# Kernel tuning notes

Measured on AMD Instinct MI355X. Metric: run time of the kernel, lower is better.

The kernel has to match this reference:

```python
import jax, jax.numpy as jnp
import numpy as np

K = 3      # kernel_size
PAD = 1    # padding


def _bilinear_gather(x, py, px, mask):
    """Modulated bilinear sampling (DCNv2 / torchvision semantics, zero padding).
    x:   [B,C,H,W]; py,px: [B,KK,H,W] float sample coords; mask: [B,KK,H,W].
    Returns [B,C,KK,H,W]."""
    B, C, H, W = x.shape
    KK = py.shape[1]
    y0f = jnp.floor(py); x0f = jnp.floor(px)
    y0 = y0f.astype(jnp.int32); x0 = x0f.astype(jnp.int32)
    wy1 = py - y0f; wx1 = px - x0f
    wy0 = 1.0 - wy1; wx0 = 1.0 - wx1
    x_flat = x.reshape(B, C, H * W)

    def corner(iy, ix, wgt):
        valid = (iy >= 0) & (iy < H) & (ix >= 0) & (ix < W)
        idx = (jnp.clip(iy, 0, H - 1) * W + jnp.clip(ix, 0, W - 1)).reshape(B, -1)
        g = jax.vmap(lambda xb, ib: jnp.take(xb, ib, axis=1))(x_flat, idx)
        g = g.reshape(B, C, KK, H, W)
        return g * (wgt * valid.astype(x.dtype))[:, None]

    val = (corner(y0, x0, wy0 * wx0)
           + corner(y0, x0 + 1, wy0 * wx1)
           + corner(y0 + 1, x0, wy1 * wx0)
           + corner(y0 + 1, x0 + 1, wy1 * wx1))
    return val * mask[:, None]


def reference(x, w_offset, b_offset, w_dcn):
    B, C, H, W = x.shape
    KK = K * K
    # offset/mask conv (stride 1, same padding)
    om = jax.lax.conv_general_dilated(
        x, w_offset, (1, 1), [(PAD, PAD), (PAD, PAD)],
        dimension_numbers=('NCHW', 'OIHW', 'NCHW')) + b_offset[None, :, None, None]
    o1, o2, m = om[:, :KK], om[:, KK:2 * KK], om[:, 2 * KK:]
    # module concatenates [o1, o2]; torchvision interprets channels as interleaved (dy, dx) pairs
    offset = jnp.concatenate([o1, o2], axis=1)          # [B, 2*KK, H, W]
    dy = offset[:, 0::2]                                # [B, KK, H, W]
    dx = offset[:, 1::2]
    mask = jax.nn.sigmoid(m)
    # base sampling grid per kernel tap
    kr = jnp.arange(K, dtype=x.dtype)
    ky = jnp.repeat(kr, K)                              # [KK]
    kx = jnp.tile(kr, K)
    by = jnp.arange(H, dtype=x.dtype)[:, None]          # [H,1]
    bx = jnp.arange(W, dtype=x.dtype)[None, :]          # [1,W]
    py = by[None, None] - PAD + ky[None, :, None, None] + dy
    px = bx[None, None] - PAD + kx[None, :, None, None] + dx
    val = _bilinear_gather(x, py, px, mask)             # [B,C,KK,H,W]
    w = w_dcn.reshape(w_dcn.shape[0], C, KK)            # [Cout, Cin, KK]
    return jnp.einsum('bckhw,ock->bohw', val, w)


def setup_inputs() -> dict:
    key = jax.random.key(0)
    k1, k2, k3, k4 = jax.random.split(key, 4)
    B, C_in, C_out, H, W = 8, 64, 64, 128, 128
    KK = K * K
    x = jax.random.normal(k1, (B, C_in, H, W), dtype=jnp.float32)
    # small nonzero offset weights so sampling positions are perturbed (module inits to 0)
    w_offset = jax.random.normal(k2, (3 * KK, C_in, K, K), dtype=jnp.float32) * 0.01
    b_offset = jax.random.normal(k3, (3 * KK,), dtype=jnp.float32) * 0.01
    fan_in = C_in * KK
    w_dcn = jax.random.normal(k4, (C_out, C_in, K, K), dtype=jnp.float32) / np.sqrt(fan_in)
    return {"x": x, "w_offset": w_offset, "b_offset": b_offset, "w_dcn": w_dcn}
```

## Files before the change

### kernel.cpp

```cpp
#include <hip/hip_runtime.h>
#include <math.h>

#define BATCH 8
#define CIN 64
#define COUT 64
#define HH 128
#define WW 128
#define HW (HH*WW)
#define TPX 64
#define KDIM 576
#define NR 5
#define NC 69
#define NSLOT (NR*NC)
#define NITEM (NSLOT*8)

typedef __attribute__((ext_vector_type(8))) short short8;
typedef __attribute__((ext_vector_type(4))) float f32x4;
typedef __attribute__((ext_vector_type(4))) unsigned int u32x4;
typedef _Float16 h2   __attribute__((ext_vector_type(2)));
typedef _Float16 h8   __attribute__((ext_vector_type(8)));

__device__ __forceinline__ short f2h(float f) {
    union { _Float16 h; short s; } u;
    u.h = (_Float16)f;
    return u.s;
}

__global__ void __launch_bounds__(256) prep_kernel(const float* __restrict__ x,
                                                   unsigned short* __restrict__ xT,
                                                   const float* __restrict__ w_dcn,
                                                   const float* __restrict__ w_off,
                                                   unsigned short* __restrict__ wt2,
                                                   unsigned short* __restrict__ wtoff2) {
    if (blockIdx.x < 4096) {
        int idx = blockIdx.x * 256 + threadIdx.x;
        int c8 = idx & 7;
        int w  = (idx >> 3) & 127;
        int h  = (idx >> 10) & 127;
        int b  = idx >> 17;
        const float* xp = x + (((size_t)(b * 64 + c8 * 8) * 128 + h) * 128 + w);
        short8 o;
#pragma unroll
        for (int j = 0; j < 8; ++j)
            o[j] = f2h(xp[(size_t)j * HW]);
        *(short8*)(xT + (size_t)idx * 8) = o;
        return;
    }
    int gid = (blockIdx.x - 4096) * 256 + threadIdx.x;
    if (gid < 72 * 64) {
        int frag = gid >> 6, lane = gid & 63;
        int kf = frag >> 3, s = (frag >> 2) & 1, m = frag & 3;
        int o = m * 16 + (lane & 15);
        int cb = s * 32 + (lane >> 4) * 8;
        short8 v;
#pragma unroll
        for (int j = 0; j < 8; ++j)
            v[j] = f2h(w_dcn[(o * 64 + cb + j) * 9 + kf]);
        *(short8*)(wt2 + (size_t)gid * 8) = v;
    } else {
        int g2 = gid - 72 * 64;
        if (g2 < 36 * 64) {
            int frag = g2 >> 6, lane = g2 & 63;
            int kk = frag >> 1, m = frag & 1;
            int kf = kk >> 1;
            int o = m * 16 + (lane & 15);
            int cb = (kk & 1) * 32 + (lane >> 4) * 8;
            short8 v;
#pragma unroll
            for (int j = 0; j < 8; ++j)
                v[j] = (o < 27) ? f2h(w_off[(o * 64 + cb + j) * 9 + kf]) : (short)0;
            *(short8*)(wtoff2 + (size_t)g2 * 8) = v;
        }
    }
}

#define LOAD_CORNERS(KF)                                                    \
    do {                                                                    \
        u32x4 e = *(const u32x4*)(s_geo8 + (size_t)(pxl * 9 + (KF)) * 16);  \
        int msk = (int)e.w >> 31;            \
        oow |= (e.w >> 31) << (KF);                                         \
        unsigned u0 = e.x & ~msk, u1 = e.y & ~msk;                          \
        union { unsigned u; h2 h; } c0_, c1_;                               \
        c0_.u = u0; c1_.u = u1;                                             \
        W0 = (h2){c0_.h.x, c0_.h.x}; W1 = (h2){c0_.h.y, c0_.h.y};           \
        W2 = (h2){c1_.h.x, c1_.h.x}; W3 = (h2){c1_.h.y, c1_.h.y};           \
        int base = (int)(e.z & ~msk);                                       \
        int sw00 = (int)(e.w & 0x70u);                                      \
        int sw01 = (int)((e.w >> 8) & 0x70u);                               \
        int sw10 = (int)((e.w >> 16) & 0x70u);                              \
        int sw11 = (int)((e.w >> 24) & 0x70u);                              \
        int q40 = g4 << 4;                                                  \
        int q41 = 64 + q40;                                                 \
        V0 = *(const h8*)(s_x + base + (q40 ^ sw00));                       \
        V1 = *(const h8*)(s_x + base + 128 + (q40 ^ sw01));                 \
        V2 = *(const h8*)(s_x + base + 8832 + (q40 ^ sw10));                \
        V3 = *(const h8*)(s_x + base + 8960 + (q40 ^ sw11));                \
        V4 = *(const h8*)(s_x + base + (q41 ^ sw00));                       \
        V5 = *(const h8*)(s_x + base + 128 + (q41 ^ sw01));                 \
        V6 = *(const h8*)(s_x + base + 8832 + (q41 ^ sw10));                \
        V7 = *(const h8*)(s_x + base + 8960 + (q41 ^ sw11));                \
    } while (0)

__global__ void __launch_bounds__(256, 3) fused_dcn_kernel(
        const unsigned short* __restrict__ xT,
        const unsigned short* __restrict__ wtoff2,
        const float* __restrict__ b_off,
        const unsigned short* __restrict__ wt2,
        float* __restrict__ out) {
    __shared__ char  s_x[NSLOT * 128];
    __shared__ float s_geo[TPX * 36];
    char* s_geo8 = (char*)s_geo;

    int t = threadIdx.x;
    int blk0 = blockIdx.x;
    int blk = (blk0 & 7) * 256 + (blk0 >> 3);
    int b = blk >> 8;
    int rem = blk & 255;
    int h = rem >> 1;
    int w0 = (rem & 1) << 6;

    int lane = t & 63;
    int wv = t >> 6;
    int l15 = lane & 15;
    int g4 = lane >> 4;
    int pxl = wv * 16 + l15;
    int wg = w0 + pxl;

    const unsigned short* xTb = xT + (size_t)b * HW * 64;

    {
        short8 v[11];
        int cs[11], cl[11];
#pragma unroll
        for (int it = 0; it < 11; ++it) {
            int i = it * 256 + t;
            if (i < NITEM) {
                int c_slot = i >> 3;
                cl[it] = i & 7;
                int r5 = c_slot / NC;
                int c  = c_slot - r5 * NC;
                cs[it] = c_slot;
                int row_src = min(max(h - 2 + r5, 0), 127);
                int col_src = min(max(w0 - 2 + c, 0), 127);
                v[it] = *(const short8*)(xTb + ((size_t)row_src * 128 + col_src) * 64 + cl[it] * 8);
            }
        }
#pragma unroll
        for (int it = 0; it < 11; ++it) {
            int i = it * 256 + t;
            if (i < NITEM) {
                int c_slot = cs[it];
                int r5 = c_slot / NC;
                int c = c_slot - r5 * NC;
                int baddr = c_slot * 128 + ((cl[it] ^ (c & 7) ^ r5) << 4);
                *(short8*)(s_x + baddr) = v[it];
            }
        }
    }
    __syncthreads();

    {
        f32x4 ca0 = {0.f, 0.f, 0.f, 0.f};
        f32x4 ca1 = {0.f, 0.f, 0.f, 0.f};
#pragma unroll
        for (int kk = 0; kk < 18; ++kk) {
            int kf = kk >> 1;
            int ky = kf / 3, kx = kf % 3;
            int cq = (kk & 1) * 4 + g4;
            int row = h - 1 + ky;
            int col = wg - 1 + kx;
            int cc = pxl + 1 + kx;
            int wr = ky + 1;
            int addr = (wr * NC + cc) * 128 + ((cq ^ (cc & 7) ^ wr) << 4);
            h8 bfrag = *(const h8*)(s_x + addr);
            if (!((unsigned)row < 128u && (unsigned)col < 128u))
                bfrag = (h8){0, 0, 0, 0, 0, 0, 0, 0};
            h8 a0 = *(const h8*)(wtoff2 + (size_t)(kk * 2 + 0) * 512 + lane * 8);
            h8 a1 = *(const h8*)(wtoff2 + (size_t)(kk * 2 + 1) * 512 + lane * 8);
            ca0 = __builtin_amdgcn_mfma_f32_16x16x32_f16(a0, bfrag, ca0, 0, 0, 0);
            ca1 = __builtin_amdgcn_mfma_f32_16x16x32_f16(a1, bfrag, ca1, 0, 0, 0);
        }
        float* gp = s_geo + pxl * 36;
        int ch0 = g4 * 4;
#pragma unroll
        for (int r = 0; r < 4; ++r) {
            int ch = ch0 + r;
            float v1 = ca0[r] + b_off[ch];
            gp[(ch >> 1) * 4 + (ch & 1)] = v1;
            int ch2 = 16 + ch;
            if (ch2 < 18) {
                float v2 = ca1[r] + b_off[ch2];
                gp[8 * 4 + (ch2 - 16)] = v2;
            } else if (ch2 < 27) {
                float v2 = ca1[r] + b_off[ch2];
                gp[(ch2 - 18) * 4 + 2] = 1.0f / (1.0f + __expf(-v2));
            }
        }
    }
    __syncthreads();

    for (int idx = t; idx < TPX * 9; idx += 256) {
        int px = idx / 9, kf = idx - (idx / 9) * 9;
        float* gp = s_geo + (size_t)idx * 4;
        float dy = gp[0], dxo = gp[1], m = gp[2];
        float py  = (float)(h - 1 + kf / 3) + dy;
        float pxf = (float)(w0 + px - 1 + kf % 3) + dxo;
        float y0f = floorf(py), x0f = floorf(pxf);
        float wy1 = py - y0f, wx1 = pxf - x0f;
        float wy0 = 1.f - wy1, wx0 = 1.f - wx1;
        int y0 = (int)y0f, x0 = (int)x0f;
        float ay0 = ((unsigned)y0 < 128u) ? wy0 * m : 0.f;
        float ay1 = ((unsigned)(y0 + 1) < 128u) ? wy1 * m : 0.f;
        float ax0 = ((unsigned)x0 < 128u) ? wx0 : 0.f;
        float ax1 = ((unsigned)(x0 + 1) < 128u) ? wx1 : 0.f;
        float w00 = ay0 * ax0, w01 = ay0 * ax1;
        float w10 = ay1 * ax0, w11 = ay1 * ax1;
        union { struct { _Float16 a, b; } s; unsigned u; } cv;
        cv.s.a = (_Float16)w00; cv.s.b = (_Float16)w01;
        unsigned uw0 = cv.u;
        cv.s.a = (_Float16)w10; cv.s.b = (_Float16)w11;
        unsigned uw1 = cv.u;
        int r50 = y0 - (h - 2);
        int c0  = x0 - (w0 - 2);
        bool inw = (r50 >= 0) & (r50 <= 3) & (c0 >= 0) & (c0 <= 67);
        unsigned wd2, wd3;
        if (inw) {
            wd2 = (unsigned)((r50 * NC + c0) * 128);
            unsigned s00 = (unsigned)(((c0 & 7) ^ (r50 & 7)) << 4);
            unsigned s01 = (unsigned)((((c0 + 1) & 7) ^ (r50 & 7)) << 4);
            unsigned s10 = (unsigned)(((c0 & 7) ^ ((r50 + 1) & 7)) << 4);
            unsigned s11 = (unsigned)((((c0 + 1) & 7) ^ ((r50 + 1) & 7)) << 4);
            wd3 = s00 | (s01 << 8) | (s10 << 16) | (s11 << 24);
        } else {
            int y0c = min(max(y0, -1), 127) + 1;
            int x0c = min(max(x0, -1), 127) + 1;
            wd2 = ((unsigned)y0c << 16) | (unsigned)x0c;
            wd3 = 0x80000000u;
        }
        unsigned* wp = (unsigned*)gp;
        wp[0] = uw0; wp[1] = uw1; wp[2] = wd2; wp[3] = wd3;
    }
    __syncthreads();

    f32x4 acc0 = {0.f, 0.f, 0.f, 0.f};
    f32x4 acc1 = {0.f, 0.f, 0.f, 0.f};
    f32x4 acc2 = {0.f, 0.f, 0.f, 0.f};
    f32x4 acc3 = {0.f, 0.f, 0.f, 0.f};

    h8 a_cur[8], a_nxt[8];
#pragma unroll
    for (int q = 0; q < 8; ++q)
        a_cur[q] = *(const h8*)(wt2 + (size_t)q * 512 + lane * 8);

    h8 V0, V1, V2, V3, V4, V5, V6, V7;
    h2 W0, W1, W2, W3;
    unsigned oow = 0;
    LOAD_CORNERS(0);

#pragma unroll
    for (int kf = 0; kf < 9; ++kf) {
        h8 bf0, bf1;
        {
            const h2* p0 = (const h2*)&V0;
            const h2* p1 = (const h2*)&V1;
            const h2* p2 = (const h2*)&V2;
            const h2* p3 = (const h2*)&V3;
            h2* bp = (h2*)&bf0;
#pragma unroll
            for (int j = 0; j < 4; ++j) {
                h2 r = p3[j] * W3;
                r = p2[j] * W2 + r;
                r = p1[j] * W1 + r;
                r = p0[j] * W0 + r;
                bp[j] = r;
            }
            const h2* q0 = (const h2*)&V4;
            const h2* q1 = (const h2*)&V5;
            const h2* q2 = (const h2*)&V6;
            const h2* q3 = (const h2*)&V7;
            h2* bq = (h2*)&bf1;
#pragma unroll
            for (int j = 0; j < 4; ++j) {
                h2 r = q3[j] * W3;
                r = q2[j] * W2 + r;
                r = q1[j] * W1 + r;
                r = q0[j] * W0 + r;
                bq[j] = r;
            }
        }

        if (kf < 8) {
            LOAD_CORNERS(kf + 1);
#pragma unroll
            for (int q = 0; q < 8; ++q)
                a_nxt[q] = *(const h8*)(wt2 + (size_t)((kf + 1) * 8 + q) * 512 + lane * 8);
        }

        __builtin_amdgcn_s_setprio(1);
        acc0 = __builtin_amdgcn_mfma_f32_16x16x32_f16(a_cur[0], bf0, acc0, 0, 0, 0);
        acc1 = __builtin_amdgcn_mfma_f32_16x16x32_f16(a_cur[1], bf0, acc1, 0, 0, 0);
        acc2 = __builtin_amdgcn_mfma_f32_16x16x32_f16(a_cur[2], bf0, acc2, 0, 0, 0);
        acc3 = __builtin_amdgcn_mfma_f32_16x16x32_f16(a_cur[3], bf0, acc3, 0, 0, 0);
        acc0 = __builtin_amdgcn_mfma_f32_16x16x32_f16(a_cur[4], bf1, acc0, 0, 0, 0);
        acc1 = __builtin_amdgcn_mfma_f32_16x16x32_f16(a_cur[5], bf1, acc1, 0, 0, 0);
        acc2 = __builtin_amdgcn_mfma_f32_16x16x32_f16(a_cur[6], bf1, acc2, 0, 0, 0);
        acc3 = __builtin_amdgcn_mfma_f32_16x16x32_f16(a_cur[7], bf1, acc3, 0, 0, 0);
        __builtin_amdgcn_s_setprio(0);

#pragma unroll
        for (int q = 0; q < 8; ++q)
            a_cur[q] = a_nxt[q];
    }

    if (__builtin_expect(__any((int)(oow != 0)), 0)) {
#pragma unroll 1
        for (int kf = 0; kf < 9; ++kf) {
            if (!__any((int)((oow >> kf) & 1u))) continue;
            u32x4 e = *(const u32x4*)(s_geo8 + (size_t)(pxl * 9 + kf) * 16);
            int keep = -(int)(e.w >> 31);
            unsigned u0 = e.x & (unsigned)keep, u1 = e.y & (unsigned)keep;
            union { unsigned u; h2 h; } c0_, c1_;
            c0_.u = u0; c1_.u = u1;
            h2 X0 = {c0_.h.x, c0_.h.x}, X1 = {c0_.h.y, c0_.h.y};
            h2 X2 = {c1_.h.x, c1_.h.x}, X3 = {c1_.h.y, c1_.h.y};
            int y0c = (int)((e.z >> 16) & 0xffu) - 1;
            int x0c = (int)(e.z & 0xffu) - 1;
            int y0a = max(y0c, 0) * 8192;
            int y1a = min(y0c + 1, 127) * 8192;
            int x0a = max(x0c, 0) * 64;
            int x1a = min(x0c + 1, 127) * 64;
            h8 af[8];
#pragma unroll
            for (int q = 0; q < 8; ++q)
                af[q] = *(const h8*)(wt2 + (size_t)(kf * 8 + q) * 512 + lane * 8);
#pragma unroll
            for (int s = 0; s < 2; ++s) {
                int cb = s * 32 + g4 * 8;
                h8 v00 = *(const h8*)(xTb + y0a + x0a + cb);
                h8 v01 = *(const h8*)(xTb + y0a + x1a + cb);
                h8 v10 = *(const h8*)(xTb + y1a + x0a + cb);
                h8 v11 = *(const h8*)(xTb + y1a + x1a + cb);
                h8 bf;
                const h2* p0 = (const h2*)&v00;
                const h2* p1 = (const h2*)&v01;
                const h2* p2 = (const h2*)&v10;
                const h2* p3 = (const h2*)&v11;
                h2* bp = (h2*)&bf;
#pragma unroll
                for (int j = 0; j < 4; ++j) {
                    h2 r = p3[j] * X3;
                    r = p2[j] * X2 + r;
                    r = p1[j] * X1 + r;
                    r = p0[j] * X0 + r;
                    bp[j] = r;
                }
                acc0 = __builtin_amdgcn_mfma_f32_16x16x32_f16(af[s * 4 + 0], bf, acc0, 0, 0, 0);
                acc1 = __builtin_amdgcn_mfma_f32_16x16x32_f16(af[s * 4 + 1], bf, acc1, 0, 0, 0);
                acc2 = __builtin_amdgcn_mfma_f32_16x16x32_f16(af[s * 4 + 2], bf, acc2, 0, 0, 0);
                acc3 = __builtin_amdgcn_mfma_f32_16x16x32_f16(af[s * 4 + 3], bf, acc3, 0, 0, 0);
            }
        }
    }

    float* obp = out + (size_t)b * COUT * HW + (size_t)h * WW + wg;
    int or0 = g4 * 4;
#pragma unroll
    for (int r = 0; r < 4; ++r) {
        obp[(size_t)(or0 + r) * HW]      = acc0[r];
        obp[(size_t)(16 + or0 + r) * HW] = acc1[r];
        obp[(size_t)(32 + or0 + r) * HW] = acc2[r];
        obp[(size_t)(48 + or0 + r) * HW] = acc3[r];
    }
}

extern "C" void kernel_launch(void* const* d_in, const int* in_sizes, int n_in,
                              void* d_out, int out_size, void* d_ws, size_t ws_size,
                              hipStream_t stream) {
    (void)in_sizes; (void)n_in; (void)out_size; (void)ws_size;
    const float* x        = (const float*)d_in[0];
    const float* w_offset = (const float*)d_in[1];
    const float* b_offset = (const float*)d_in[2];
    const float* w_dcn    = (const float*)d_in[3];
    float* out = (float*)d_out;

    unsigned short* xT     = (unsigned short*)d_ws;
    unsigned short* wt2    = (unsigned short*)((char*)d_ws + 16777216);
    unsigned short* wtoff2 = (unsigned short*)((char*)d_ws + 16850944);

    prep_kernel<<<4096 + 27, 256, 0, stream>>>(x, xT, w_dcn, w_offset, wt2, wtoff2);
    fused_dcn_kernel<<<2048, 256, 0, stream>>>(xT, wtoff2, b_offset, wt2, out);
}
```

Baseline: 55.61 us.

## Transpose x via swizzled LDS tile in prep and prefetch geometry entries earlier

The NCHW-to-NHWC fp16 transpose in the prep kernel now does vectorized float4 reads along W per channel. It stages the tile in a swizzled shared-memory buffer, then writes 16-byte channel vectors, which replaces the previous strided scalar reads. The block count is halved because each block now covers 64 pixels by 64 channels. In the fused kernel, each per-tap geometry entry is read from LDS one tap ahead, so that LDS read latency is hidden behind the corner loads. The cost is an extra shared-memory buffer plus a barrier in prep, and a few more live registers in the main loop.

```diff
diff --git a/kernel.cpp b/kernel.cpp
--- a/kernel.cpp
+++ b/kernel.cpp
@@ -32,21 +32,42 @@
                                                    const float* __restrict__ w_off,
                                                    unsigned short* __restrict__ wt2,
                                                    unsigned short* __restrict__ wtoff2) {
-    if (blockIdx.x < 4096) {
-        int idx = blockIdx.x * 256 + threadIdx.x;
-        int c8 = idx & 7;
-        int w  = (idx >> 3) & 127;
-        int h  = (idx >> 10) & 127;
-        int b  = idx >> 17;
-        const float* xp = x + (((size_t)(b * 64 + c8 * 8) * 128 + h) * 128 + w);
-        short8 o;
-#pragma unroll
-        for (int j = 0; j < 8; ++j)
-            o[j] = f2h(xp[(size_t)j * HW]);
-        *(short8*)(xT + (size_t)idx * 8) = o;
+    __shared__ unsigned short s_t[4096];
+    int blk = blockIdx.x;
+    int t = threadIdx.x;
+    if (blk < 2048) {
+        int b = blk >> 8;
+        int hw = blk & 255;
+        int h = hw >> 1;
+        int w0 = (hw & 1) << 6;
+        int c = t & 63;
+        int seg = t >> 6;
+        int c8 = c >> 3;
+        const float* xp = x + (((size_t)(b * 64 + c) * 128 + h) * 128 + w0 + seg * 16);
+        f32x4 A0 = *(const f32x4*)(xp);
+        f32x4 A1 = *(const f32x4*)(xp + 4);
+        f32x4 A2 = *(const f32x4*)(xp + 8);
+        f32x4 A3 = *(const f32x4*)(xp + 12);
+        float vals[16] = {A0[0],A0[1],A0[2],A0[3], A1[0],A1[1],A1[2],A1[3],
+                          A2[0],A2[1],A2[2],A2[3], A3[0],A3[1],A3[2],A3[3]};
+#pragma unroll
+        for (int j = 0; j < 16; ++j) {
+            int wl = seg * 16 + j;
+            s_t[wl * 64 + ((c8 ^ (wl & 7)) * 8) + (c & 7)] = (unsigned short)f2h(vals[j]);
+        }
+        __syncthreads();
+        unsigned short* xo = xT + (size_t)b * HW * 64 + ((size_t)h * 128 + w0) * 64;
+#pragma unroll
+        for (int uu = 0; uu < 2; ++uu) {
+            int u = uu * 256 + t;
+            int w = u >> 3;
+            int cc8 = u & 7;
+            short8 v = *(const short8*)(s_t + w * 64 + ((cc8 ^ (w & 7)) * 8));
+            *(short8*)(xo + (size_t)w * 64 + cc8 * 8) = v;
+        }
         return;
     }
-    int gid = (blockIdx.x - 4096) * 256 + threadIdx.x;
+    int gid = (blk - 2048) * 256 + t;
     if (gid < 72 * 64) {
         int frag = gid >> 6, lane = gid & 63;
         int kf = frag >> 3, s = (frag >> 2) & 1, m = frag & 3;
@@ -74,21 +95,23 @@
     }
 }
 
-#define LOAD_CORNERS(KF)                                                    \
+#define READ_ENTRY(KF, E)                                                   \
+    E = *(const u32x4*)(s_geo8 + (size_t)(pxl * 9 + (KF)) * 16)
+
+#define CORNERS_FROM(E, KF)                                                 \
     do {                                                                    \
-        u32x4 e = *(const u32x4*)(s_geo8 + (size_t)(pxl * 9 + (KF)) * 16);  \
-        int msk = (int)e.w >> 31;            \
-        oow |= (e.w >> 31) << (KF);                                         \
-        unsigned u0 = e.x & ~msk, u1 = e.y & ~msk;                          \
+        int msk = (int)E.w >> 31;            \
+        oow |= (E.w >> 31) << (KF);                                         \
+        unsigned u0 = E.x & ~msk, u1 = E.y & ~msk;                          \
         union { unsigned u; h2 h; } c0_, c1_;                               \
         c0_.u = u0; c1_.u = u1;                                             \
         W0 = (h2){c0_.h.x, c0_.h.x}; W1 = (h2){c0_.h.y, c0_.h.y};           \
         W2 = (h2){c1_.h.x, c1_.h.x}; W3 = (h2){c1_.h.y, c1_.h.y};           \
-        int base = (int)(e.z & ~msk);                                       \
-        int sw00 = (int)(e.w & 0x70u);                                      \
-        int sw01 = (int)((e.w >> 8) & 0x70u);                               \
-        int sw10 = (int)((e.w >> 16) & 0x70u);                              \
-        int sw11 = (int)((e.w >> 24) & 0x70u);                              \
+        int base = (int)(E.z & ~msk);                                       \
+        int sw00 = (int)(E.w & 0x70u);                                      \
+        int sw01 = (int)((E.w >> 8) & 0x70u);                               \
+        int sw10 = (int)((E.w >> 16) & 0x70u);                              \
+        int sw11 = (int)((E.w >> 24) & 0x70u);                              \
         int q40 = g4 << 4;                                                  \
         int q41 = 64 + q40;                                                 \
         V0 = *(const h8*)(s_x + base + (q40 ^ sw00));                       \
@@ -255,7 +278,10 @@
     h8 V0, V1, V2, V3, V4, V5, V6, V7;
     h2 W0, W1, W2, W3;
     unsigned oow = 0;
-    LOAD_CORNERS(0);
+    u32x4 e_cur, e_nxt;
+    READ_ENTRY(0, e_cur);
+    CORNERS_FROM(e_cur, 0);
+    READ_ENTRY(1, e_nxt);
 
 #pragma unroll
     for (int kf = 0; kf < 9; ++kf) {
@@ -290,7 +316,8 @@
         }
 
         if (kf < 8) {
-            LOAD_CORNERS(kf + 1);
+            CORNERS_FROM(e_nxt, kf + 1);
+            if (kf < 7) { READ_ENTRY(kf + 2, e_nxt); }
 #pragma unroll
             for (int q = 0; q < 8; ++q)
                 a_nxt[q] = *(const h8*)(wt2 + (size_t)((kf + 1) * 8 + q) * 512 + lane * 8);
@@ -387,6 +414,6 @@
     unsigned short* wt2    = (unsigned short*)((char*)d_ws + 16777216);
     unsigned short* wtoff2 = (unsigned short*)((char*)d_ws + 16850944);
 
-    prep_kernel<<<4096 + 27, 256, 0, stream>>>(x, xT, w_dcn, w_offset, wt2, wtoff2);
+    prep_kernel<<<2048 + 27, 256, 0, stream>>>(x, xT, w_dcn, w_offset, wt2, wtoff2);
     fused_dcn_kernel<<<2048, 256, 0, stream>>>(xT, wtoff2, b_offset, wt2, out);
 }
```

New measurement: 53.20 us (median of 2 runs). 1.05x faster.
